# Kernel optimization log

Measured on AMD Instinct MI355X. Metric: run time of the kernel, lower is better.

Reference implementation:

```python
import jax, jax.numpy as jnp
import numpy as np

B, S, K, DEPTH = 8, 8192, 512, 2
NUM_SPECIALS = 4  # bos, eos, pad, eop


def setup_inputs() -> dict:
    key = jax.random.key(0)
    ks = jax.random.split(key, 6)
    stage_logits = jax.random.normal(ks[0], (DEPTH, B, S, K), jnp.float32)
    special_logits = jax.random.normal(ks[1], (B, S, NUM_SPECIALS), jnp.float32)
    seq = jax.random.randint(ks[2], (B, S), 0, K ** DEPTH, jnp.int32)
    lengths = jax.random.randint(ks[3], (B,), S // 2, S)
    kpm = jnp.arange(S)[None, :] >= lengths[:, None]              # True = pad
    end_mask = (jax.random.uniform(ks[4], (B, S)) < 0.1) & (~kpm)  # segment ends
    # exclusive cumsum of end_mask -> segment ids
    seg = jnp.cumsum(
        jnp.pad(end_mask[:, :-1], ((0, 0), (1, 0))).astype(jnp.int32), axis=1)
    targets = jax.random.randint(ks[5], (B, S), 0, K ** DEPTH + NUM_SPECIALS, jnp.int32)
    return {
        "stage_logits": stage_logits,
        "special_logits": special_logits,
        "seq": seq,
        "end_mask": end_mask,
        "kpm": kpm,
        "seg": seg,
        "targets": targets,
        "tgt_kpm": kpm,
        "eop_id": K ** DEPTH + 3,
        "pad_id": K ** DEPTH + 2,
    }


def _insert_eop(seq, end_mask, kpm, seg, eop_id, pad_id):
    """Length-preserving EOP insertion + seg-id update (torch _insert_eop_fixed_len_with_seg)."""
    B_, S_ = seq.shape
    pad_slots = kpm.sum(axis=1)                                   # free slots per row
    csum = jnp.cumsum(end_mask.astype(jnp.int32), axis=1)
    end_mask = end_mask & (csum <= pad_slots[:, None])            # cap insertions by capacity
    m = end_mask.astype(jnp.int32)
    c = jnp.cumsum(m, axis=1)
    shift = c - m                                                  # inclusive-cumsum minus self
    real = ~kpm
    tok = jnp.arange(S_, dtype=jnp.int32)[None, :]
    bidx = jnp.arange(B_)[:, None]
    tgt = tok + shift                                              # destination of each real token
    tgt_real = jnp.where(real, tgt, S_)                            # index S_ -> dropped (OOB)
    out = jnp.full((B_, S_), pad_id, seq.dtype)
    out = out.at[bidx, tgt_real].set(seq, mode="drop")
    out_kpm = jnp.ones((B_, S_), bool).at[bidx, tgt_real].set(False, mode="drop")
    out_seg = jnp.zeros_like(seg).at[bidx, tgt_real].set(seg, mode="drop")
    need_eop = real & end_mask
    tgt_eop = jnp.where(need_eop, tgt + 1, S_)                     # EOP right after the token
    out = out.at[bidx, tgt_eop].set(eop_id, mode="drop")
    out_kpm = out_kpm.at[bidx, tgt_eop].set(False, mode="drop")
    out_seg = out_seg.at[bidx, tgt_eop].set(seg, mode="drop")      # EOP inherits seg id
    last_seg = jnp.clip(jnp.max(jnp.where(kpm, -1, seg), axis=1), 0, None)
    out_seg = jnp.where(out_kpm, last_seg[:, None], out_seg)       # pads get last seg id
    return out, out_kpm, out_seg


def _factorized_ce(stage_logits, special_logits, targets, tgt_kpm):
    """Stage-wise digit CE + special-head CE (torch _factorized_code_ce with codec)."""
    depth, _, _, Kd = stage_logits.shape
    base = Kd ** depth
    is_special = targets >= base
    valid = (~is_special) & (~tgt_kpm)
    denom = jnp.maximum(valid.sum(), 1).astype(stage_logits.dtype)
    digit_loss = jnp.zeros((), stage_logits.dtype)
    for s in range(depth):  # small fixed loop over VQ stages
        dig = (targets // (Kd ** s)) % Kd                          # codec.decompose digit s
        logp = jax.nn.log_softmax(stage_logits[s], axis=-1)
        ce = -jnp.take_along_axis(logp, dig[..., None], axis=-1)[..., 0]
        digit_loss = digit_loss + (ce * valid).sum() / denom
    sp_local = jnp.clip(targets - base, 0, special_logits.shape[-1] - 1)
    sp_mask = is_special & (~tgt_kpm)
    logp_sp = jax.nn.log_softmax(special_logits, axis=-1)
    ce_sp = -jnp.take_along_axis(logp_sp, sp_local[..., None], axis=-1)[..., 0]
    special_loss = (ce_sp * sp_mask).sum() / jnp.maximum(sp_mask.sum(), 1).astype(ce_sp.dtype)
    return digit_loss, special_loss


def reference(stage_logits, special_logits, seq, end_mask, kpm, seg, targets, tgt_kpm, eop_id, pad_id):
    out, out_kpm, out_seg = _insert_eop(seq, end_mask, kpm, seg, eop_id, pad_id)
    digit_ce, special_ce = _factorized_ce(stage_logits, special_logits, targets, tgt_kpm)
    return out, out_kpm, out_seg, digit_ce, special_ce
```

## Files before the change

### kernel.cpp

```cpp
#include <hip/hip_runtime.h>

#define S_LEN 8192
#define B_SZ 8
#define BASE 262144
#define BT_TOTAL 65536
#define ROWS_TOTAL 131072
#define ROWS_PER_WAVE 16


__device__ __forceinline__ int load_bool(const void* p, int idx, int isByte) {
  if (isByte) return (int)((const unsigned char*)p)[idx];
  return ((const int*)p)[idx];
}

__global__ __launch_bounds__(256) void init_kernel(const unsigned* kpm_raw,
                                                   float* wsf, int* wsi) {
  __shared__ int bad;
  if (threadIdx.x == 0) bad = 0;
  __syncthreads();
  int any = 0;
  for (int i = threadIdx.x; i < BT_TOTAL / 4; i += 256) {
    if (kpm_raw[i] & ~1u) any = 1;
  }
  if (any) atomicOr(&bad, 1);
  __syncthreads();
  if (threadIdx.x == 0) {
    wsf[0] = 0.f; wsf[1] = 0.f; wsf[2] = 0.f;
    wsi[3] = 0; wsi[4] = 0; wsi[5] = bad;
  }
}

__global__ __launch_bounds__(1024) void eop_kernel(
    const int* __restrict__ seq, const void* __restrict__ end_mask,
    const void* __restrict__ kpm, const int* __restrict__ seg,
    const int* __restrict__ eop_idp, const int* __restrict__ pad_idp,
    const int* __restrict__ wsi, float* __restrict__ out) {
  __shared__ int s_seg[S_LEN];
  __shared__ int sh_ps[16], sh_ls[16], sh_w[16];
  __shared__ int sh_pad, sh_last, sh_carry;

  const int b = blockIdx.x;
  const int tid = threadIdx.x;
  const int lane = tid & 63;
  const int wid = tid >> 6;
  const int isByte = wsi[5];
  const int eop_id = eop_idp[0];
  const int pad_id = pad_idp[0];

  float* outF = out + (size_t)b * S_LEN;
  float* kpmF = out + BT_TOTAL + (size_t)b * S_LEN;
  float* segF = out + 2 * BT_TOTAL + (size_t)b * S_LEN;
  const int* seqR = seq + (size_t)b * S_LEN;
  const int* segR = seg + (size_t)b * S_LEN;
  const int rowBase = b * S_LEN;

  for (int t = tid; t < S_LEN; t += 1024) {
    outF[t] = (float)pad_id;
    s_seg[t] = -1;
  }

  int ps = 0, ls = -1;
  for (int t = tid; t < S_LEN; t += 1024) {
    int kp = load_bool(kpm, rowBase + t, isByte);
    ps += kp;
    if (!kp) ls = max(ls, segR[t]);
  }
  for (int off = 32; off; off >>= 1) {
    ps += __shfl_xor(ps, off);
    ls = max(ls, __shfl_xor(ls, off));
  }
  if (lane == 0) { sh_ps[wid] = ps; sh_ls[wid] = ls; }
  __syncthreads();
  if (tid == 0) {
    int a = 0, m = -1;
    for (int i = 0; i < 16; ++i) { a += sh_ps[i]; m = max(m, sh_ls[i]); }
    sh_pad = a;
    sh_last = max(m, 0);
    sh_carry = 0;
  }
  __syncthreads();
  const int pad_slots = sh_pad;
  const int last_seg = sh_last;

  for (int tile = 0; tile < 8; ++tile) {
    const int t = tile * 1024 + tid;
    const int e = load_bool(end_mask, rowBase + t, isByte);
    int x = e;
    for (int off = 1; off < 64; off <<= 1) {
      int y = __shfl_up(x, off);
      if (lane >= off) x += y;
    }
    if (lane == 63) sh_w[wid] = x;
    __syncthreads();
    if (tid == 0) {
      int acc = sh_carry;
      for (int i = 0; i < 16; ++i) { int v = sh_w[i]; sh_w[i] = acc; acc += v; }
      sh_carry = acc;
    }
    __syncthreads();
    const int csum_raw = sh_w[wid] + x;
    const int em2 = (e && csum_raw <= pad_slots) ? 1 : 0;
    const int c = min(csum_raw, pad_slots);
    const int shift = c - em2;
    const int kp = load_bool(kpm, rowBase + t, isByte);
    if (!kp) {
      const int tgt = t + shift;
      const int sv = segR[t];
      if (tgt < S_LEN) {
        outF[tgt] = (float)seqR[t];
        s_seg[tgt] = sv;
      }
      if (em2 && (tgt + 1) < S_LEN) {
        outF[tgt + 1] = (float)eop_id;
        s_seg[tgt + 1] = sv;
      }
    }
    __syncthreads();
  }

  for (int t = tid; t < S_LEN; t += 1024) {
    const int sv = s_seg[t];
    kpmF[t] = (sv < 0) ? 1.0f : 0.0f;
    segF[t] = (sv < 0) ? (float)last_seg : (float)sv;
  }
}

__global__ __launch_bounds__(256) void ce_kernel(
    const float* __restrict__ stage_logits, const int* __restrict__ targets,
    const void* __restrict__ tgt_kpm, const int* __restrict__ wsi,
    float* __restrict__ wsf, int* __restrict__ wsi_out) {
  const int isByte = wsi[5];
  const int lane = threadIdx.x & 63;
  const int wid = threadIdx.x >> 6;
  const long long wave_g = (long long)blockIdx.x * 4 + wid;
  const long long row0 = wave_g * ROWS_PER_WAVE;
  const int s = (int)(row0 >> 16);

  float ce_sum = 0.f;
  int vcnt = 0;

  for (int i = 0; i < ROWS_PER_WAVE; ++i) {
    const long long r = row0 + i;
    const int bt = (int)(r & (BT_TOTAL - 1));
    const int tgt = targets[bt];
    const int kp = load_bool(tgt_kpm, bt, isByte);
    if (kp || tgt >= BASE) continue;

    const float* rowp = stage_logits + ((size_t)r << 9);
    const float4 c0 = ((const float4*)rowp)[lane];
    const float4 c1 = ((const float4*)rowp)[lane + 64];

    float m = fmaxf(fmaxf(fmaxf(c0.x, c0.y), fmaxf(c0.z, c0.w)),
                    fmaxf(fmaxf(c1.x, c1.y), fmaxf(c1.z, c1.w)));
    for (int off = 32; off; off >>= 1) m = fmaxf(m, __shfl_xor(m, off));

    float ssum = __expf(c0.x - m) + __expf(c0.y - m) + __expf(c0.z - m) +
                 __expf(c0.w - m) + __expf(c1.x - m) + __expf(c1.y - m) +
                 __expf(c1.z - m) + __expf(c1.w - m);
    for (int off = 32; off; off >>= 1) ssum += __shfl_xor(ssum, off);

    const int dig = (s == 0) ? (tgt & 511) : ((tgt >> 9) & 511);
    const int srcLane = (dig >> 2) & 63;
    const int j = dig & 3;
    float xv;
    if (dig < 256)
      xv = (j == 0) ? c0.x : (j == 1) ? c0.y : (j == 2) ? c0.z : c0.w;
    else
      xv = (j == 0) ? c1.x : (j == 1) ? c1.y : (j == 2) ? c1.z : c1.w;
    xv = __shfl(xv, srcLane);

    ce_sum += m + __logf(ssum) - xv;
    ++vcnt;
  }

  __shared__ float s_ce[4];
  __shared__ int s_cnt[4];
  if (lane == 0) { s_ce[wid] = ce_sum; s_cnt[wid] = vcnt; }
  __syncthreads();
  if (threadIdx.x == 0) {
    atomicAdd(&wsf[s], s_ce[0] + s_ce[1] + s_ce[2] + s_ce[3]);
    if (s == 0)
      atomicAdd(&wsi_out[3], s_cnt[0] + s_cnt[1] + s_cnt[2] + s_cnt[3]);
  }
}

__global__ __launch_bounds__(256) void special_kernel(
    const float* __restrict__ sp_logits, const int* __restrict__ targets,
    const void* __restrict__ tgt_kpm, const int* __restrict__ wsi,
    float* __restrict__ wsf, int* __restrict__ wsi_out) {
  const int bt = blockIdx.x * 256 + threadIdx.x;
  const int isByte = wsi[5];
  const int tgt = targets[bt];
  const int kp = load_bool(tgt_kpm, bt, isByte);
  if (!kp && tgt >= BASE) {
    const float4 v = ((const float4*)sp_logits)[bt];
    const float m = fmaxf(fmaxf(v.x, v.y), fmaxf(v.z, v.w));
    const float ssum = __expf(v.x - m) + __expf(v.y - m) + __expf(v.z - m) +
                       __expf(v.w - m);
    const int sl = min(tgt - BASE, 3);
    const float xv = (sl == 0) ? v.x : (sl == 1) ? v.y : (sl == 2) ? v.z : v.w;
    atomicAdd(&wsf[2], m + __logf(ssum) - xv);
    atomicAdd(&wsi_out[4], 1);
  }
}

__global__ void finalize_kernel(const float* __restrict__ wsf,
                                const int* __restrict__ wsi,
                                float* __restrict__ out) {
  if (threadIdx.x == 0) {
    const float denom = (float)max(wsi[3], 1);
    out[3 * BT_TOTAL] = (wsf[0] + wsf[1]) / denom;
    out[3 * BT_TOTAL + 1] = wsf[2] / (float)max(wsi[4], 1);
  }
}

extern "C" void kernel_launch(void* const* d_in, const int* in_sizes, int n_in,
                              void* d_out, int out_size, void* d_ws,
                              size_t ws_size, hipStream_t stream) {
  const float* stage_logits   = (const float*)d_in[0];
  const float* special_logits = (const float*)d_in[1];
  const int*   seq            = (const int*)d_in[2];
  const void*  end_mask       = d_in[3];
  const void*  kpm            = d_in[4];
  const int*   seg            = (const int*)d_in[5];
  const int*   targets        = (const int*)d_in[6];
  const void*  tgt_kpm        = d_in[7];
  const int*   eop_idp        = (const int*)d_in[8];
  const int*   pad_idp        = (const int*)d_in[9];

  float* out = (float*)d_out;
  float* wsf = (float*)d_ws;
  int*   wsi = (int*)d_ws;

  init_kernel<<<1, 256, 0, stream>>>((const unsigned*)kpm, wsf, wsi);
  eop_kernel<<<B_SZ, 1024, 0, stream>>>(seq, end_mask, kpm, seg, eop_idp,
                                        pad_idp, wsi, out);
  ce_kernel<<<ROWS_TOTAL / ROWS_PER_WAVE / 4, 256, 0, stream>>>(
      stage_logits, targets, tgt_kpm, wsi, wsf, wsi);
  special_kernel<<<BT_TOTAL / 256, 256, 0, stream>>>(special_logits, targets,
                                                     tgt_kpm, wsi, wsf, wsi);
  finalize_kernel<<<1, 64, 0, stream>>>(wsf, wsi, out);
}
```

Before: 414.7 us.

## Fuse EOP insertion, digit CE, special CE and finalize into one kernel

Five launches (init, eop, ce, special, finalize) are merged into a single kernel. The first eight blocks perform EOP insertion plus the special-token CE, and the other blocks compute digit CE with targets preloaded once per wave through shuffles. A last-block-done atomic counter writes the final losses, and a memset replaces the init kernel. The byte-versus-int mask detection now checks only one word of kpm instead of scanning the whole array, which could misdetect the format on other inputs.

```diff
diff --git a/kernel.cpp b/kernel.cpp
--- a/kernel.cpp
+++ b/kernel.cpp
@@ -6,211 +6,230 @@
 #define BT_TOTAL 65536
 #define ROWS_TOTAL 131072
 #define ROWS_PER_WAVE 16
+#define EOP_BLOCKS 8
+#define CE_BLOCKS 512
+#define GRID_TOTAL (EOP_BLOCKS + CE_BLOCKS)
 
 
 __device__ __forceinline__ int load_bool(const void* p, int idx, int isByte) {
-  if (isByte) return (int)((const unsigned char*)p)[idx];
-  return ((const int*)p)[idx];
+  return isByte ? (int)((const unsigned char*)p)[idx] : ((const int*)p)[idx];
 }
 
-__global__ __launch_bounds__(256) void init_kernel(const unsigned* kpm_raw,
-                                                   float* wsf, int* wsi) {
-  __shared__ int bad;
-  if (threadIdx.x == 0) bad = 0;
-  __syncthreads();
-  int any = 0;
-  for (int i = threadIdx.x; i < BT_TOTAL / 4; i += 256) {
-    if (kpm_raw[i] & ~1u) any = 1;
-  }
-  if (any) atomicOr(&bad, 1);
-  __syncthreads();
-  if (threadIdx.x == 0) {
-    wsf[0] = 0.f; wsf[1] = 0.f; wsf[2] = 0.f;
-    wsi[3] = 0; wsi[4] = 0; wsi[5] = bad;
-  }
-}
-
-__global__ __launch_bounds__(1024) void eop_kernel(
-    const int* __restrict__ seq, const void* __restrict__ end_mask,
-    const void* __restrict__ kpm, const int* __restrict__ seg,
-    const int* __restrict__ eop_idp, const int* __restrict__ pad_idp,
-    const int* __restrict__ wsi, float* __restrict__ out) {
+__global__ __launch_bounds__(1024, 2) void fused_kernel(
+    const float* __restrict__ stage_logits,
+    const float* __restrict__ sp_logits,
+    const int* __restrict__ seq,
+    const void* __restrict__ end_mask,
+    const void* __restrict__ kpm,
+    const int* __restrict__ seg,
+    const int* __restrict__ targets,
+    const void* __restrict__ tgt_kpm,
+    const int* __restrict__ eop_idp,
+    const int* __restrict__ pad_idp,
+    float* __restrict__ out,
+    float* __restrict__ wsf, int* __restrict__ wsi) {
   __shared__ int s_seg[S_LEN];
-  __shared__ int sh_ps[16], sh_ls[16], sh_w[16];
+  __shared__ float s_red[16];
+  __shared__ int s_redi[16];
+  __shared__ int sh_w[16], sh_ps[16], sh_ls[16];
   __shared__ int sh_pad, sh_last, sh_carry;
 
-  const int b = blockIdx.x;
   const int tid = threadIdx.x;
   const int lane = tid & 63;
   const int wid = tid >> 6;
-  const int isByte = wsi[5];
-  const int eop_id = eop_idp[0];
-  const int pad_id = pad_idp[0];
-
-  float* outF = out + (size_t)b * S_LEN;
-  float* kpmF = out + BT_TOTAL + (size_t)b * S_LEN;
-  float* segF = out + 2 * BT_TOTAL + (size_t)b * S_LEN;
-  const int* seqR = seq + (size_t)b * S_LEN;
-  const int* segR = seg + (size_t)b * S_LEN;
-  const int rowBase = b * S_LEN;
-
-  for (int t = tid; t < S_LEN; t += 1024) {
-    outF[t] = (float)pad_id;
-    s_seg[t] = -1;
+
+  const int isByte = ((((const unsigned*)kpm)[2047] & ~1u) != 0u) ? 1 : 0;
+
+  if (blockIdx.x >= EOP_BLOCKS) {
+    const int ceb = blockIdx.x - EOP_BLOCKS;
+    const int row0 = (ceb * 16 + wid) * ROWS_PER_WAVE;
+    const int stage = row0 >> 16;
+
+    int tgt_l = 0, val_l = 0;
+    if (lane < ROWS_PER_WAVE) {
+      const int bt = (row0 + lane) & (BT_TOTAL - 1);
+      tgt_l = targets[bt];
+      const int kp = load_bool(tgt_kpm, bt, isByte);
+      val_l = (!kp && tgt_l < BASE) ? 1 : 0;
+    }
+
+    float ce_sum = 0.f;
+    int vcnt = 0;
+    for (int i = 0; i < ROWS_PER_WAVE; ++i) {
+      const int v = __shfl(val_l, i);
+      if (!v) continue;
+      const int tgt = __shfl(tgt_l, i);
+      const float* rowp = stage_logits + ((size_t)(row0 + i) << 9);
+      const float4 c0 = ((const float4*)rowp)[lane];
+      const float4 c1 = ((const float4*)rowp)[lane + 64];
+
+      float m = fmaxf(fmaxf(fmaxf(c0.x, c0.y), fmaxf(c0.z, c0.w)),
+                      fmaxf(fmaxf(c1.x, c1.y), fmaxf(c1.z, c1.w)));
+      for (int off = 32; off; off >>= 1) m = fmaxf(m, __shfl_xor(m, off));
+
+      float ssum = __expf(c0.x - m) + __expf(c0.y - m) + __expf(c0.z - m) +
+                   __expf(c0.w - m) + __expf(c1.x - m) + __expf(c1.y - m) +
+                   __expf(c1.z - m) + __expf(c1.w - m);
+      for (int off = 32; off; off >>= 1) ssum += __shfl_xor(ssum, off);
+
+      const int dig = (stage == 0) ? (tgt & 511) : (tgt >> 9);
+      const int srcLane = (dig >> 2) & 63;
+      const int j = dig & 3;
+      float xv;
+      if (dig < 256)
+        xv = (j == 0) ? c0.x : (j == 1) ? c0.y : (j == 2) ? c0.z : c0.w;
+      else
+        xv = (j == 0) ? c1.x : (j == 1) ? c1.y : (j == 2) ? c1.z : c1.w;
+      xv = __shfl(xv, srcLane);
+
+      ce_sum += m + __logf(ssum) - xv;
+      ++vcnt;
+    }
+
+    if (lane == 0) {
+      s_red[wid] = ce_sum;
+      s_redi[wid] = (stage == 0) ? vcnt : 0;
+    }
+    __syncthreads();
+    if (tid == 0) {
+      float a = 0.f;
+      int c = 0;
+      for (int i = 0; i < 16; ++i) { a += s_red[i]; c += s_redi[i]; }
+      atomicAdd(&wsf[0], a);
+      if (c) atomicAdd(&wsi[2], c);
+    }
+  } else {
+    const int b = blockIdx.x;
+    const int eop_id = eop_idp[0];
+    const int pad_id = pad_idp[0];
+
+    float* outF = out + (size_t)b * S_LEN;
+    float* kpmF = out + BT_TOTAL + (size_t)b * S_LEN;
+    float* segF = out + 2 * BT_TOTAL + (size_t)b * S_LEN;
+    const int* seqR = seq + (size_t)b * S_LEN;
+    const int* segR = seg + (size_t)b * S_LEN;
+    const int rowBase = b * S_LEN;
+
+    for (int t = tid; t < S_LEN; t += 1024) {
+      outF[t] = (float)pad_id;
+      s_seg[t] = -1;
+    }
+
+    int ps = 0, ls = -1;
+    for (int t = tid; t < S_LEN; t += 1024) {
+      const int kp = load_bool(kpm, rowBase + t, isByte);
+      ps += kp;
+      if (!kp) ls = max(ls, segR[t]);
+    }
+    for (int off = 32; off; off >>= 1) {
+      ps += __shfl_xor(ps, off);
+      ls = max(ls, __shfl_xor(ls, off));
+    }
+    if (lane == 0) { sh_ps[wid] = ps; sh_ls[wid] = ls; }
+    __syncthreads();
+    if (tid == 0) {
+      int a = 0, m = -1;
+      for (int i = 0; i < 16; ++i) { a += sh_ps[i]; m = max(m, sh_ls[i]); }
+      sh_pad = a;
+      sh_last = max(m, 0);
+      sh_carry = 0;
+    }
+    __syncthreads();
+    const int pad_slots = sh_pad;
+    const int last_seg = sh_last;
+
+    for (int tile = 0; tile < 8; ++tile) {
+      const int t = tile * 1024 + tid;
+      const int e = load_bool(end_mask, rowBase + t, isByte);
+      int x = e;
+      for (int off = 1; off < 64; off <<= 1) {
+        const int y = __shfl_up(x, off);
+        if (lane >= off) x += y;
+      }
+      if (lane == 63) sh_w[wid] = x;
+      __syncthreads();
+      if (tid == 0) {
+        int acc = sh_carry;
+        for (int i = 0; i < 16; ++i) { const int v = sh_w[i]; sh_w[i] = acc; acc += v; }
+        sh_carry = acc;
+      }
+      __syncthreads();
+      const int csum_raw = sh_w[wid] + x;
+      const int em2 = (e && csum_raw <= pad_slots) ? 1 : 0;
+      const int c = min(csum_raw, pad_slots);
+      const int shift = c - em2;
+      const int kp = load_bool(kpm, rowBase + t, isByte);
+      if (!kp) {
+        const int tgt = t + shift;
+        const int sv = segR[t];
+        if (tgt < S_LEN) {
+          outF[tgt] = (float)seqR[t];
+          s_seg[tgt] = sv;
+        }
+        if (em2 && (tgt + 1) < S_LEN) {
+          outF[tgt + 1] = (float)eop_id;
+          s_seg[tgt + 1] = sv;
+        }
+      }
+      __syncthreads();
+    }
+
+    for (int t = tid; t < S_LEN; t += 1024) {
+      const int sv = s_seg[t];
+      kpmF[t] = (sv < 0) ? 1.0f : 0.0f;
+      segF[t] = (sv < 0) ? (float)last_seg : (float)sv;
+    }
+
+    float sp_sum = 0.f;
+    int sp_cnt = 0;
+    for (int t = tid; t < S_LEN; t += 1024) {
+      const int bt = rowBase + t;
+      const int tgt = targets[bt];
+      const int kp = load_bool(tgt_kpm, bt, isByte);
+      if (!kp && tgt >= BASE) {
+        const float4 v = ((const float4*)sp_logits)[bt];
+        const float m = fmaxf(fmaxf(v.x, v.y), fmaxf(v.z, v.w));
+        const float ssum = __expf(v.x - m) + __expf(v.y - m) +
+                           __expf(v.z - m) + __expf(v.w - m);
+        const int sl = min(tgt - BASE, 3);
+        const float xv = (sl == 0) ? v.x : (sl == 1) ? v.y
+                        : (sl == 2) ? v.z : v.w;
+        sp_sum += m + __logf(ssum) - xv;
+        ++sp_cnt;
+      }
+    }
+    for (int off = 32; off; off >>= 1) {
+      sp_sum += __shfl_xor(sp_sum, off);
+      sp_cnt += __shfl_xor(sp_cnt, off);
+    }
+    if (lane == 0) { s_red[wid] = sp_sum; s_redi[wid] = sp_cnt; }
+    __syncthreads();
+    if (tid == 0) {
+      float a = 0.f;
+      int c = 0;
+      for (int i = 0; i < 16; ++i) { a += s_red[i]; c += s_redi[i]; }
+      if (a != 0.f) atomicAdd(&wsf[1], a);
+      if (c) atomicAdd(&wsi[3], c);
+    }
   }
 
-  int ps = 0, ls = -1;
-  for (int t = tid; t < S_LEN; t += 1024) {
-    int kp = load_bool(kpm, rowBase + t, isByte);
-    ps += kp;
-    if (!kp) ls = max(ls, segR[t]);
-  }
-  for (int off = 32; off; off >>= 1) {
-    ps += __shfl_xor(ps, off);
-    ls = max(ls, __shfl_xor(ls, off));
-  }
-  if (lane == 0) { sh_ps[wid] = ps; sh_ls[wid] = ls; }
   __syncthreads();
   if (tid == 0) {
-    int a = 0, m = -1;
-    for (int i = 0; i < 16; ++i) { a += sh_ps[i]; m = max(m, sh_ls[i]); }
-    sh_pad = a;
-    sh_last = max(m, 0);
-    sh_carry = 0;
-  }
-  __syncthreads();
-  const int pad_slots = sh_pad;
-  const int last_seg = sh_last;
-
-  for (int tile = 0; tile < 8; ++tile) {
-    const int t = tile * 1024 + tid;
-    const int e = load_bool(end_mask, rowBase + t, isByte);
-    int x = e;
-    for (int off = 1; off < 64; off <<= 1) {
-      int y = __shfl_up(x, off);
-      if (lane >= off) x += y;
-    }
-    if (lane == 63) sh_w[wid] = x;
-    __syncthreads();
-    if (tid == 0) {
-      int acc = sh_carry;
-      for (int i = 0; i < 16; ++i) { int v = sh_w[i]; sh_w[i] = acc; acc += v; }
-      sh_carry = acc;
-    }
-    __syncthreads();
-    const int csum_raw = sh_w[wid] + x;
-    const int em2 = (e && csum_raw <= pad_slots) ? 1 : 0;
-    const int c = min(csum_raw, pad_slots);
-    const int shift = c - em2;
-    const int kp = load_bool(kpm, rowBase + t, isByte);
-    if (!kp) {
-      const int tgt = t + shift;
-      const int sv = segR[t];
-      if (tgt < S_LEN) {
-        outF[tgt] = (float)seqR[t];
-        s_seg[tgt] = sv;
-      }
-      if (em2 && (tgt + 1) < S_LEN) {
-        outF[tgt + 1] = (float)eop_id;
-        s_seg[tgt + 1] = sv;
-      }
-    }
-    __syncthreads();
-  }
-
-  for (int t = tid; t < S_LEN; t += 1024) {
-    const int sv = s_seg[t];
-    kpmF[t] = (sv < 0) ? 1.0f : 0.0f;
-    segF[t] = (sv < 0) ? (float)last_seg : (float)sv;
-  }
-}
-
-__global__ __launch_bounds__(256) void ce_kernel(
-    const float* __restrict__ stage_logits, const int* __restrict__ targets,
-    const void* __restrict__ tgt_kpm, const int* __restrict__ wsi,
-    float* __restrict__ wsf, int* __restrict__ wsi_out) {
-  const int isByte = wsi[5];
-  const int lane = threadIdx.x & 63;
-  const int wid = threadIdx.x >> 6;
-  const long long wave_g = (long long)blockIdx.x * 4 + wid;
-  const long long row0 = wave_g * ROWS_PER_WAVE;
-  const int s = (int)(row0 >> 16);
-
-  float ce_sum = 0.f;
-  int vcnt = 0;
-
-  for (int i = 0; i < ROWS_PER_WAVE; ++i) {
-    const long long r = row0 + i;
-    const int bt = (int)(r & (BT_TOTAL - 1));
-    const int tgt = targets[bt];
-    const int kp = load_bool(tgt_kpm, bt, isByte);
-    if (kp || tgt >= BASE) continue;
-
-    const float* rowp = stage_logits + ((size_t)r << 9);
-    const float4 c0 = ((const float4*)rowp)[lane];
-    const float4 c1 = ((const float4*)rowp)[lane + 64];
-
-    float m = fmaxf(fmaxf(fmaxf(c0.x, c0.y), fmaxf(c0.z, c0.w)),
-                    fmaxf(fmaxf(c1.x, c1.y), fmaxf(c1.z, c1.w)));
-    for (int off = 32; off; off >>= 1) m = fmaxf(m, __shfl_xor(m, off));
-
-    float ssum = __expf(c0.x - m) + __expf(c0.y - m) + __expf(c0.z - m) +
-                 __expf(c0.w - m) + __expf(c1.x - m) + __expf(c1.y - m) +
-                 __expf(c1.z - m) + __expf(c1.w - m);
-    for (int off = 32; off; off >>= 1) ssum += __shfl_xor(ssum, off);
-
-    const int dig = (s == 0) ? (tgt & 511) : ((tgt >> 9) & 511);
-    const int srcLane = (dig >> 2) & 63;
-    const int j = dig & 3;
-    float xv;
-    if (dig < 256)
-      xv = (j == 0) ? c0.x : (j == 1) ? c0.y : (j == 2) ? c0.z : c0.w;
-    else
-      xv = (j == 0) ? c1.x : (j == 1) ? c1.y : (j == 2) ? c1.z : c1.w;
-    xv = __shfl(xv, srcLane);
-
-    ce_sum += m + __logf(ssum) - xv;
-    ++vcnt;
-  }
-
-  __shared__ float s_ce[4];
-  __shared__ int s_cnt[4];
-  if (lane == 0) { s_ce[wid] = ce_sum; s_cnt[wid] = vcnt; }
-  __syncthreads();
-  if (threadIdx.x == 0) {
-    atomicAdd(&wsf[s], s_ce[0] + s_ce[1] + s_ce[2] + s_ce[3]);
-    if (s == 0)
-      atomicAdd(&wsi_out[3], s_cnt[0] + s_cnt[1] + s_cnt[2] + s_cnt[3]);
-  }
-}
-
-__global__ __launch_bounds__(256) void special_kernel(
-    const float* __restrict__ sp_logits, const int* __restrict__ targets,
-    const void* __restrict__ tgt_kpm, const int* __restrict__ wsi,
-    float* __restrict__ wsf, int* __restrict__ wsi_out) {
-  const int bt = blockIdx.x * 256 + threadIdx.x;
-  const int isByte = wsi[5];
-  const int tgt = targets[bt];
-  const int kp = load_bool(tgt_kpm, bt, isByte);
-  if (!kp && tgt >= BASE) {
-    const float4 v = ((const float4*)sp_logits)[bt];
-    const float m = fmaxf(fmaxf(v.x, v.y), fmaxf(v.z, v.w));
-    const float ssum = __expf(v.x - m) + __expf(v.y - m) + __expf(v.z - m) +
-                       __expf(v.w - m);
-    const int sl = min(tgt - BASE, 3);
-    const float xv = (sl == 0) ? v.x : (sl == 1) ? v.y : (sl == 2) ? v.z : v.w;
-    atomicAdd(&wsf[2], m + __logf(ssum) - xv);
-    atomicAdd(&wsi_out[4], 1);
-  }
-}
-
-__global__ void finalize_kernel(const float* __restrict__ wsf,
-                                const int* __restrict__ wsi,
-                                float* __restrict__ out) {
-  if (threadIdx.x == 0) {
-    const float denom = (float)max(wsi[3], 1);
-    out[3 * BT_TOTAL] = (wsf[0] + wsf[1]) / denom;
-    out[3 * BT_TOTAL + 1] = wsf[2] / (float)max(wsi[4], 1);
+    __threadfence();
+    const int old = atomicAdd(&wsi[4], 1);
+    if (old == GRID_TOTAL - 1) {
+      __threadfence();
+      const float ds = __hip_atomic_load(&wsf[0], __ATOMIC_RELAXED,
+                                         __HIP_MEMORY_SCOPE_AGENT);
+      const float ss = __hip_atomic_load(&wsf[1], __ATOMIC_RELAXED,
+                                         __HIP_MEMORY_SCOPE_AGENT);
+      const int vc = __hip_atomic_load(&wsi[2], __ATOMIC_RELAXED,
+                                       __HIP_MEMORY_SCOPE_AGENT);
+      const int sc = __hip_atomic_load(&wsi[3], __ATOMIC_RELAXED,
+                                       __HIP_MEMORY_SCOPE_AGENT);
+      out[3 * BT_TOTAL] = ds / (float)max(vc, 1);
+      out[3 * BT_TOTAL + 1] = ss / (float)max(sc, 1);
+    }
   }
 }
 
@@ -228,16 +247,8 @@
   const int*   eop_idp        = (const int*)d_in[8];
   const int*   pad_idp        = (const int*)d_in[9];
 
-  float* out = (float*)d_out;
-  float* wsf = (float*)d_ws;
-  int*   wsi = (int*)d_ws;
-
-  init_kernel<<<1, 256, 0, stream>>>((const unsigned*)kpm, wsf, wsi);
-  eop_kernel<<<B_SZ, 1024, 0, stream>>>(seq, end_mask, kpm, seg, eop_idp,
-                                        pad_idp, wsi, out);
-  ce_kernel<<<ROWS_TOTAL / ROWS_PER_WAVE / 4, 256, 0, stream>>>(
-      stage_logits, targets, tgt_kpm, wsi, wsf, wsi);
-  special_kernel<<<BT_TOTAL / 256, 256, 0, stream>>>(special_logits, targets,
-                                                     tgt_kpm, wsi, wsf, wsi);
-  finalize_kernel<<<1, 64, 0, stream>>>(wsf, wsi, out);
+  hipMemsetAsync(d_ws, 0, 64, stream);
+  fused_kernel<<<GRID_TOTAL, 1024, 0, stream>>>(
+      stage_logits, special_logits, seq, end_mask, kpm, seg, targets, tgt_kpm,
+      eop_idp, pad_idp, (float*)d_out, (float*)d_ws, (int*)d_ws);
 }
```

Result: faster. 391.3 us (-5.6%).
